# Optimization experiments

Measured on AMD Instinct MI355X. Metric: run time of the kernel, lower is better.

## Reference

```python
import jax, jax.numpy as jnp
import numpy as np

B, N, CH, DIM, SLOTS, ITERS, HID = 32, 4096, 256, 256, 11, 3, 512
EPS_ATTN = 1e-8
LN_EPS = 1e-3


def _ln(x, g, b):
    m = jnp.mean(x, axis=-1, keepdims=True)
    v = jnp.mean((x - m) ** 2, axis=-1, keepdims=True)
    return (x - m) * jax.lax.rsqrt(v + LN_EPS) * g + b


def setup_inputs() -> dict:
    key = jax.random.key(0)
    ks = jax.random.split(key, 16)
    s = lambda d: 1.0 / np.sqrt(d)
    return {
        "inputs": jax.random.normal(ks[0], (B, N, CH), jnp.float32),
        "noise": jax.random.normal(ks[1], (B, SLOTS, DIM), jnp.float32),
        "slots_mu": jax.random.uniform(ks[2], (1, 1, DIM), jnp.float32, -0.15, 0.15),
        "slots_log_sigma": jax.random.uniform(ks[3], (1, 1, DIM), jnp.float32, -0.15, 0.15),
        "Wq": jax.random.normal(ks[4], (DIM, DIM), jnp.float32) * s(DIM),
        "Wk": jax.random.normal(ks[5], (DIM, CH), jnp.float32) * s(CH),
        "Wv": jax.random.normal(ks[6], (DIM, CH), jnp.float32) * s(CH),
        "W_ih": jax.random.normal(ks[7], (3 * DIM, DIM), jnp.float32) * s(DIM),
        "W_hh": jax.random.normal(ks[8], (3 * DIM, DIM), jnp.float32) * s(DIM),
        "b_ih": jnp.zeros((3 * DIM,), jnp.float32),
        "b_hh": jnp.zeros((3 * DIM,), jnp.float32),
        "W1": jax.random.normal(ks[9], (HID, DIM), jnp.float32) * s(DIM),
        "b1": jnp.zeros((HID,), jnp.float32),
        "W2": jax.random.normal(ks[10], (DIM, HID), jnp.float32) * s(HID),
        "b2": jnp.zeros((DIM,), jnp.float32),
        "g_in": jnp.ones((CH,), jnp.float32), "be_in": jnp.zeros((CH,), jnp.float32),
        "g_sl": jnp.ones((DIM,), jnp.float32), "be_sl": jnp.zeros((DIM,), jnp.float32),
        "g_ff": jnp.ones((DIM,), jnp.float32), "be_ff": jnp.zeros((DIM,), jnp.float32),
    }


def reference(inputs, noise, slots_mu, slots_log_sigma, Wq, Wk, Wv, W_ih, W_hh,
              b_ih, b_hh, W1, b1, W2, b2, g_in, be_in, g_sl, be_sl, g_ff, be_ff):
    scale = DIM ** -0.5
    # reparameterized slot init: Normal(mu, exp(log_sigma))
    slots = slots_mu + jnp.exp(slots_log_sigma) * noise  # (B, S, D)
    x = _ln(inputs, g_in, be_in)
    k = jnp.einsum('bnc,dc->bnd', x, Wk)  # (B, N, D)
    v = jnp.einsum('bnc,dc->bnd', x, Wv)

    def gru(u, h):
        gi = u @ W_ih.T + b_ih
        gh = h @ W_hh.T + b_hh
        i_r, i_z, i_n = jnp.split(gi, 3, axis=-1)
        h_r, h_z, h_n = jnp.split(gh, 3, axis=-1)
        r = jax.nn.sigmoid(i_r + h_r)
        z = jax.nn.sigmoid(i_z + h_z)
        n = jnp.tanh(i_n + r * h_n)
        return (1.0 - z) * n + z * h

    for _ in range(ITERS):
        slots_prev = slots
        q = jnp.einsum('bid,ed->bie', _ln(slots, g_sl, be_sl), Wq)
        dots = jnp.einsum('bid,bjd->bij', q, k) * scale  # (B, S, N)
        attn = jax.nn.softmax(dots, axis=1) + EPS_ATTN   # competitive over slots
        attn = attn / jnp.sum(attn, axis=-1, keepdims=True)
        updates = jnp.einsum('bjd,bij->bid', v, attn)    # (B, S, D)
        slots = gru(updates.reshape(-1, DIM), slots_prev.reshape(-1, DIM)).reshape(B, -1, DIM)
        h = jax.nn.relu(_ln(slots, g_ff, be_ff) @ W1.T + b1)
        slots = slots + h @ W2.T + b2
    return slots
```

## Files before the change

kernel.cpp:

```cpp
#include <hip/hip_runtime.h>
#include <hip/hip_bf16.h>
#include <math.h>

typedef __bf16 bf16;
typedef __bf16 bf16x8 __attribute__((ext_vector_type(8)));
typedef float  f32x4  __attribute__((ext_vector_type(4)));

#define DEVI static __device__ __forceinline__

constexpr int B_ = 32, N_ = 4096, NS_ = 11, SP_ = 16, ITERS_ = 3;
constexpr int P_ = 32;
constexpr float LN_EPS_ = 1e-3f;
constexpr float EPS_ATTN_ = 1e-8f;

DEVI f32x4 mfma16(bf16x8 a, bf16x8 b, f32x4 c) {
  return __builtin_amdgcn_mfma_f32_16x16x32_bf16(a, b, c, 0, 0, 0);
}

DEVI float wsum64(float v) {
#pragma unroll
  for (int m = 32; m > 0; m >>= 1) v += __shfl_xor(v, m, 64);
  return v;
}

__global__ __launch_bounds__(256) void cast_weights(
    const float* __restrict__ Wq, const float* __restrict__ Wk,
    const float* __restrict__ Wv, const float* __restrict__ Wih,
    const float* __restrict__ Whh, const float* __restrict__ W1,
    const float* __restrict__ W2,
    bf16* __restrict__ cWkT, bf16* __restrict__ cWvT, bf16* __restrict__ cWq,
    bf16* __restrict__ cWih, bf16* __restrict__ cWhh, bf16* __restrict__ cW1,
    bf16* __restrict__ cW2) {
  const int idx = blockIdx.x * 256 + threadIdx.x;
  const int n0 = 256 * 256;
  const int n1 = n0 + 256 * 256;
  const int n2 = n1 + 256 * 256;
  const int n3 = n2 + 768 * 256;
  const int n4 = n3 + 768 * 256;
  const int n5 = n4 + 512 * 256;
  const int n6 = n5 + 256 * 512;
  if (idx < n0) {
    const int c = idx >> 8, d = idx & 255;
    cWkT[idx] = (bf16)Wk[d * 256 + c];
  } else if (idx < n1) {
    const int i = idx - n0; const int c = i >> 8, d = i & 255;
    cWvT[i] = (bf16)Wv[d * 256 + c];
  } else if (idx < n2) { const int i = idx - n1; cWq[i]  = (bf16)Wq[i];
  } else if (idx < n3) { const int i = idx - n2; cWih[i] = (bf16)Wih[i];
  } else if (idx < n4) { const int i = idx - n3; cWhh[i] = (bf16)Whh[i];
  } else if (idx < n5) { const int i = idx - n4; cW1[i]  = (bf16)W1[i];
  } else if (idx < n6) { const int i = idx - n5; cW2[i]  = (bf16)W2[i]; }
}

__global__ __launch_bounds__(256) void wfold_gemm(
    const bf16* __restrict__ Wih, const bf16* __restrict__ WvT,
    bf16* __restrict__ Wfold) {
  __shared__ bf16 At[32 * 256];
  const int mt = blockIdx.x, nt = blockIdx.y;
  const int tid = threadIdx.x, lane = tid & 63, wid = tid >> 6;
  const int l15 = lane & 15, gq = lane >> 4;
  const bf16* A = Wih + (size_t)mt * 32 * 256;
#pragma unroll
  for (int i = 0; i < 4; ++i) {
    const int idx = i * 256 + tid, row = idx >> 5, c = idx & 31;
    const bf16x8 v = *(const bf16x8*)(A + row * 256 + c * 8);
    const int byte = (row * 512 + c * 16) ^ ((row & 7) << 4);
    *(bf16x8*)((char*)At + byte) = v;
  }
  __syncthreads();
  const int wr = wid >> 1, wc = wid & 1;
  f32x4 acc[2] = {};
  for (int kk = 0; kk < 8; ++kk) {
    const int arow = wr * 16 + l15;
    const int byte = (arow * 512 + kk * 64 + gq * 16) ^ ((arow & 7) << 4);
    const bf16x8 af = *(const bf16x8*)((const char*)At + byte);
#pragma unroll
    for (int nn = 0; nn < 2; ++nn) {
      const bf16* wrow = WvT + (size_t)(nt * 64 + wc * 32 + nn * 16 + l15) * 256 + kk * 32 + gq * 8;
      acc[nn] = mfma16(af, *(const bf16x8*)wrow, acc[nn]);
    }
  }
#pragma unroll
  for (int nn = 0; nn < 2; ++nn)
#pragma unroll
    for (int r = 0; r < 4; ++r) {
      const int grow = mt * 32 + wr * 16 + gq * 4 + r;
      const int col = nt * 64 + wc * 32 + nn * 16 + l15;
      Wfold[(size_t)grow * 256 + col] = (bf16)acc[nn][r];
    }
}

__global__ __launch_bounds__(256) void init_slots(
    const float* __restrict__ mu, const float* __restrict__ lsig,
    const float* __restrict__ noise, float* __restrict__ slots,
    bf16* __restrict__ slots_bf) {
  const int idx = blockIdx.x * 256 + threadIdx.x;
  const int d = idx & 255;
  const float v = mu[d] + expf(lsig[d]) * noise[idx];
  slots[idx] = v;
  slots_bf[idx] = (bf16)v;
}

__global__ __launch_bounds__(256) void ln_castT(
    const float* __restrict__ inp, const float* __restrict__ g,
    const float* __restrict__ be, bf16* __restrict__ xhat,
    bf16* __restrict__ xhatT) {
  __shared__ bf16 Bt[256 * 128];
  const int mt = blockIdx.x;
  const int tid = threadIdx.x, lane = tid & 63, wid = tid >> 6;
  const int l15 = lane & 15, gq = lane >> 4;
  float4 gv[4], bv4[4];
#pragma unroll
  for (int u = 0; u < 4; ++u) {
    gv[u]  = ((const float4*)g)[l15 * 4 + u];
    bv4[u] = ((const float4*)be)[l15 * 4 + u];
  }
  const int c0 = l15 * 16;
  char* btlane = (char*)Bt + c0 * 256;
  for (int it8 = 0; it8 < 8; ++it8) {
    const int row = wid * 32 + it8 * 4 + gq;
    const size_t grow = (size_t)mt * 128 + row;
    const float4* rp = (const float4*)(inp + grow * 256 + l15 * 16);
    float4 x[4];
#pragma unroll
    for (int u = 0; u < 4; ++u) x[u] = rp[u];
    float s = 0.f, ss = 0.f;
#pragma unroll
    for (int u = 0; u < 4; ++u) {
      s += x[u].x + x[u].y + x[u].z + x[u].w;
      ss = fmaf(x[u].x, x[u].x, fmaf(x[u].y, x[u].y,
           fmaf(x[u].z, x[u].z, fmaf(x[u].w, x[u].w, ss))));
    }
#pragma unroll
    for (int m = 8; m > 0; m >>= 1) {
      s  += __shfl_xor(s,  m, 16);
      ss += __shfl_xor(ss, m, 16);
    }
    const float mean = s * (1.f / 256.f);
    const float rstd = rsqrtf(ss * (1.f / 256.f) - mean * mean + LN_EPS_);
    float y[16];
#pragma unroll
    for (int u = 0; u < 4; ++u) {
      y[u * 4 + 0] = (x[u].x - mean) * rstd * gv[u].x + bv4[u].x;
      y[u * 4 + 1] = (x[u].y - mean) * rstd * gv[u].y + bv4[u].y;
      y[u * 4 + 2] = (x[u].z - mean) * rstd * gv[u].z + bv4[u].z;
      y[u * 4 + 3] = (x[u].w - mean) * rstd * gv[u].w + bv4[u].w;
    }
    bf16x8 y0, y1;
#pragma unroll
    for (int e = 0; e < 8; ++e) { y0[e] = (bf16)y[e]; y1[e] = (bf16)y[8 + e]; }
    bf16* orow = xhat + grow * 256 + c0;
    *(bf16x8*)orow       = y0;
    *(bf16x8*)(orow + 8) = y1;
    const int roff = (row * 2) ^ c0;
#pragma unroll
    for (int j = 0; j < 8; ++j) {
      *(bf16*)(btlane + j * 256 + roff)         = y0[j];
      *(bf16*)(btlane + (8 + j) * 256 + roff)   = y1[j];
    }
  }
  __syncthreads();
  const int bidx = mt >> 5, jtile = (mt & 31) * 128;
#pragma unroll
  for (int i = 0; i < 16; ++i) {
    const int idx = i * 256 + tid;
    const int c = idx >> 4, j8 = (idx & 15) * 8;
    const bf16x8 v = *(const bf16x8*)((const char*)Bt +
                                      (c * 256 + ((j8 * 2) ^ (c & 0xF0))));
    *(bf16x8*)&xhatT[((size_t)(bidx * 256 + c)) * N_ + jtile + j8] = v;
  }
}

__global__ __launch_bounds__(256) void q_proj(
    const float* __restrict__ slots, const float* __restrict__ g,
    const float* __restrict__ be, const bf16* __restrict__ Wqb,
    const bf16* __restrict__ WkT, bf16* __restrict__ qpad) {
  const int i = blockIdx.x, b = blockIdx.y, t = threadIdx.x;
  bf16* out = qpad + (b * SP_ + i) * 256;
  if (i >= NS_) { out[t] = (bf16)0.f; return; }
  __shared__ float lnv[256], qd[256];
  __shared__ float red[8];
  const float x = slots[(b * NS_ + i) * 256 + t];
  float s = wsum64(x), ss = wsum64(x * x);
  const int lane = t & 63, w = t >> 6;
  if (lane == 0) { red[w] = s; red[4 + w] = ss; }
  __syncthreads();
  const float st = red[0] + red[1] + red[2] + red[3];
  const float qt = red[4] + red[5] + red[6] + red[7];
  const float mean = st / 256.f, var = qt / 256.f - mean * mean;
  const float rstd = rsqrtf(var + LN_EPS_);
  lnv[t] = (x - mean) * rstd * g[t] + be[t];
  __syncthreads();
  {
    float acc = 0.f;
    const bf16* wr = Wqb + (size_t)t * 256;
    for (int it = 0; it < 32; ++it) {
      const bf16x8 wv = *(const bf16x8*)(wr + it * 8);
      const float* u = &lnv[it * 8];
#pragma unroll
      for (int e = 0; e < 8; ++e) acc += (float)wv[e] * u[e];
    }
    qd[t] = acc;
  }
  __syncthreads();
  {
    float acc = 0.f;
    const bf16* wr = WkT + (size_t)t * 256;
    for (int it = 0; it < 32; ++it) {
      const bf16x8 wv = *(const bf16x8*)(wr + it * 8);
      const float* u = &qd[it * 8];
#pragma unroll
      for (int e = 0; e < 8; ++e) acc += (float)wv[e] * u[e];
    }
    out[t] = (bf16)(acc * 0.0625f);
  }
}

__global__ __launch_bounds__(256) void attn_part(
    const bf16* __restrict__ xhat, const bf16* __restrict__ xhatT,
    const bf16* __restrict__ qpad,
    float* __restrict__ num_part, float* __restrict__ den_part) {
  const int part = blockIdx.x, b = blockIdx.y;
  const int lane = threadIdx.x & 63, wid = threadIdx.x >> 6;
  const int l15 = lane & 15, gq = lane >> 4;
  const int jbase = part * 128 + wid * 32;
  const bf16* qrow = qpad + ((size_t)(b * SP_ + l15)) * 256;
  const bf16* kbase = xhat + ((size_t)(b * N_ + jbase)) * 256;
  const bf16* vtb = xhatT + ((size_t)b * 256) * N_ + jbase + gq * 8;
  __shared__ float nsw[2][4096];
  __shared__ float dens[4][16];

  bf16x8 bq[8];
#pragma unroll
  for (int kk = 0; kk < 8; ++kk)
    bq[kk] = *(const bf16x8*)(qrow + kk * 32 + gq * 8);
  bf16x8 v0[8];
#pragma unroll
  for (int dblk = 0; dblk < 8; ++dblk)
    v0[dblk] = *(const bf16x8*)(vtb + (size_t)(dblk * 16 + l15) * N_);

  float denacc = 0.f;
  float p0[4], p1[4];
#pragma unroll
  for (int T = 0; T < 2; ++T) {
    const bf16* krow = kbase + (size_t)(T * 16 + l15) * 256;
    f32x4 d = {0.f, 0.f, 0.f, 0.f};
#pragma unroll
    for (int kk = 0; kk < 8; ++kk) {
      const bf16x8 ak = *(const bf16x8*)(krow + kk * 32 + gq * 8);
      d = mfma16(ak, bq[kk], d);
    }
#pragma unroll
    for (int r = 0; r < 4; ++r) {
      float vmax = (l15 < NS_) ? d[r] : -1e30f;
#pragma unroll
      for (int mm = 8; mm > 0; mm >>= 1) vmax = fmaxf(vmax, __shfl_xor(vmax, mm, 16));
      const float e = (l15 < NS_) ? expf(d[r] - vmax) : 0.f;
      float ssum = e;
#pragma unroll
      for (int mm = 8; mm > 0; mm >>= 1) ssum += __shfl_xor(ssum, mm, 16);
      const float p = (l15 < NS_) ? (e / ssum + EPS_ATTN_) : 0.f;
      if (T == 0) p0[r] = p; else p1[r] = p;
      denacc += p;
    }
  }
  bf16x8 v1[8];
#pragma unroll
  for (int dblk = 0; dblk < 8; ++dblk)
    v1[dblk] = *(const bf16x8*)(vtb + (size_t)((8 + dblk) * 16 + l15) * N_);
  bf16x8 ap;
#pragma unroll
  for (int e = 0; e < 8; ++e) {
    const int srcl = l15 + ((2 * (gq & 1) + (e >> 2)) << 4);
    const float va = __shfl(p0[e & 3], srcl, 64);
    const float vb = __shfl(p1[e & 3], srcl, 64);
    ap[e] = (bf16)((gq < 2) ? va : vb);
  }
  f32x4 accN[16];
  __builtin_amdgcn_s_setprio(1);
#pragma unroll
  for (int dblk = 0; dblk < 8; ++dblk) {
    f32x4 z = {0.f, 0.f, 0.f, 0.f};
    accN[dblk] = mfma16(ap, v0[dblk], z);
  }
#pragma unroll
  for (int dblk = 0; dblk < 8; ++dblk) {
    f32x4 z = {0.f, 0.f, 0.f, 0.f};
    accN[8 + dblk] = mfma16(ap, v1[dblk], z);
  }
  __builtin_amdgcn_s_setprio(0);
  if (wid < 2) {
#pragma unroll
    for (int dblk = 0; dblk < 16; ++dblk)
#pragma unroll
      for (int r = 0; r < 4; ++r) {
        const int idx = (((4 * gq + r) * 256) + dblk * 16 + l15) ^ (gq << 4);
        nsw[wid][idx] = accN[dblk][r];
      }
  }
  __syncthreads();
  if (wid >= 2) {
#pragma unroll
    for (int dblk = 0; dblk < 16; ++dblk)
#pragma unroll
      for (int r = 0; r < 4; ++r) {
        const int idx = (((4 * gq + r) * 256) + dblk * 16 + l15) ^ (gq << 4);
        nsw[wid - 2][idx] += accN[dblk][r];
      }
  }
  float dtot = denacc + __shfl_xor(denacc, 16, 64);
  dtot += __shfl_xor(dtot, 32, 64);
  if (lane < 16) dens[wid][l15] = dtot;
  __syncthreads();
  const int t = threadIdx.x;
  if (t < NS_)
    den_part[(b * P_ + part) * NS_ + t] =
        dens[0][t] + dens[1][t] + dens[2][t] + dens[3][t];
  for (int r = 0; r < NS_; ++r) {
    const int swz = ((r >> 2) & 3) << 4;
    num_part[((size_t)((b * P_ + part) * NS_ + r)) * 256 + t] =
        nsw[0][(r * 256 + t) ^ swz] + nsw[1][(r * 256 + t) ^ swz];
  }
}

__global__ __launch_bounds__(256) void u0_reduce(
    const float* __restrict__ num_part, const float* __restrict__ den_part,
    bf16* __restrict__ u0b) {
  const int row = blockIdx.x, t = threadIdx.x;
  const int b = row / NS_, i = row % NS_;
  float nsum = 0.f;
  for (int p = 0; p < P_; ++p)
    nsum += num_part[((size_t)((b * P_ + p) * NS_ + i)) * 256 + t];
  float den = 0.f;
  for (int p = 0; p < P_; ++p) den += den_part[(b * P_ + p) * NS_ + i];
  u0b[(size_t)row * 256 + t] = (bf16)(nsum / den);
}

__global__ __launch_bounds__(256) void gates_gemm(
    const bf16* __restrict__ u0b, const bf16* __restrict__ hb,
    const bf16* __restrict__ Wfold, const bf16* __restrict__ Whh,
    float* __restrict__ gi, float* __restrict__ gh) {
  __shared__ bf16 At[32 * 256];
  const int mt = blockIdx.x, nt = blockIdx.y;
  const bool isI = nt < 12;
  const int ntile = isI ? nt : nt - 12;
  const bf16* A = (isI ? u0b : hb) + (size_t)mt * 32 * 256;
  const bf16* W = isI ? Wfold : Whh;
  float* out = isI ? gi : gh;
  const int tid = threadIdx.x, lane = tid & 63, wid = tid >> 6;
  const int l15 = lane & 15, gq = lane >> 4;
#pragma unroll
  for (int i = 0; i < 4; ++i) {
    const int idx = i * 256 + tid, row = idx >> 5, c = idx & 31;
    const bf16x8 v = *(const bf16x8*)(A + row * 256 + c * 8);
    const int byte = (row * 512 + c * 16) ^ ((row & 7) << 4);
    *(bf16x8*)((char*)At + byte) = v;
  }
  __syncthreads();
  const int wr = wid >> 1, wc = wid & 1;
  f32x4 acc[2] = {};
  for (int kk = 0; kk < 8; ++kk) {
    const int arow = wr * 16 + l15;
    const int byte = (arow * 512 + kk * 64 + gq * 16) ^ ((arow & 7) << 4);
    const bf16x8 af = *(const bf16x8*)((const char*)At + byte);
#pragma unroll
    for (int nn = 0; nn < 2; ++nn) {
      const bf16* wrow = W + (size_t)(ntile * 64 + wc * 32 + nn * 16 + l15) * 256 + kk * 32 + gq * 8;
      acc[nn] = mfma16(af, *(const bf16x8*)wrow, acc[nn]);
    }
  }
#pragma unroll
  for (int nn = 0; nn < 2; ++nn)
#pragma unroll
    for (int r = 0; r < 4; ++r) {
      const int grow = mt * 32 + wr * 16 + gq * 4 + r;
      const int col = ntile * 64 + wc * 32 + nn * 16 + l15;
      out[(size_t)grow * 768 + col] = acc[nn][r];
    }
}

__global__ __launch_bounds__(256) void gru_ew(
    const float* __restrict__ gi, const float* __restrict__ gh,
    const float* __restrict__ bih, const float* __restrict__ bhh,
    const float* __restrict__ slots_f, const float* __restrict__ gff,
    const float* __restrict__ beff, float* __restrict__ hn_out,
    bf16* __restrict__ ln_out) {
  const int row = blockIdx.x, t = threadIdx.x;
  __shared__ float red[8];
  const size_t g0 = (size_t)row * 768;
  const float ir = gi[g0 + t]       + bih[t];
  const float hr = gh[g0 + t]       + bhh[t];
  const float iz = gi[g0 + 256 + t] + bih[256 + t];
  const float hz = gh[g0 + 256 + t] + bhh[256 + t];
  const float inn = gi[g0 + 512 + t] + bih[512 + t];
  const float hnn = gh[g0 + 512 + t] + bhh[512 + t];
  const float h = slots_f[(size_t)row * 256 + t];
  const float r = 1.f / (1.f + expf(-(ir + hr)));
  const float z = 1.f / (1.f + expf(-(iz + hz)));
  const float n = tanhf(inn + r * hnn);
  const float hn = (1.f - z) * n + z * h;
  hn_out[(size_t)row * 256 + t] = hn;
  float s = wsum64(hn), ss = wsum64(hn * hn);
  const int lane = t & 63, w = t >> 6;
  if (lane == 0) { red[w] = s; red[4 + w] = ss; }
  __syncthreads();
  const float st = red[0] + red[1] + red[2] + red[3];
  const float qt = red[4] + red[5] + red[6] + red[7];
  const float mean = st / 256.f, var = qt / 256.f - mean * mean;
  const float rstd = rsqrtf(var + LN_EPS_);
  ln_out[(size_t)row * 256 + t] = (bf16)((hn - mean) * rstd * gff[t] + beff[t]);
}

__global__ __launch_bounds__(256) void w1_gemm(
    const bf16* __restrict__ lnb, const bf16* __restrict__ W1,
    const float* __restrict__ b1, bf16* __restrict__ h1b) {
  __shared__ bf16 At[32 * 256];
  const int mt = blockIdx.x, nt = blockIdx.y;
  const int tid = threadIdx.x, lane = tid & 63, wid = tid >> 6;
  const int l15 = lane & 15, gq = lane >> 4;
  const bf16* A = lnb + (size_t)mt * 32 * 256;
#pragma unroll
  for (int i = 0; i < 4; ++i) {
    const int idx = i * 256 + tid, row = idx >> 5, c = idx & 31;
    const bf16x8 v = *(const bf16x8*)(A + row * 256 + c * 8);
    const int byte = (row * 512 + c * 16) ^ ((row & 7) << 4);
    *(bf16x8*)((char*)At + byte) = v;
  }
  __syncthreads();
  const int wr = wid >> 1, wc = wid & 1;
  f32x4 acc[2] = {};
  for (int kk = 0; kk < 8; ++kk) {
    const int arow = wr * 16 + l15;
    const int byte = (arow * 512 + kk * 64 + gq * 16) ^ ((arow & 7) << 4);
    const bf16x8 af = *(const bf16x8*)((const char*)At + byte);
#pragma unroll
    for (int nn = 0; nn < 2; ++nn) {
      const bf16* wrow = W1 + (size_t)(nt * 64 + wc * 32 + nn * 16 + l15) * 256 + kk * 32 + gq * 8;
      acc[nn] = mfma16(af, *(const bf16x8*)wrow, acc[nn]);
    }
  }
#pragma unroll
  for (int nn = 0; nn < 2; ++nn)
#pragma unroll
    for (int r = 0; r < 4; ++r) {
      const int grow = mt * 32 + wr * 16 + gq * 4 + r;
      const int col = nt * 64 + wc * 32 + nn * 16 + l15;
      h1b[(size_t)grow * 512 + col] = (bf16)fmaxf(acc[nn][r] + b1[col], 0.f);
    }
}

__global__ __launch_bounds__(256) void w2_gemm(
    const bf16* __restrict__ h1b, const bf16* __restrict__ W2,
    const float* __restrict__ b2, const float* __restrict__ hn_in,
    float* __restrict__ sout, bf16* __restrict__ sbf) {
  __shared__ bf16 At[32 * 512];
  const int mt = blockIdx.x, nt = blockIdx.y;
  const int tid = threadIdx.x, lane = tid & 63, wid = tid >> 6;
  const int l15 = lane & 15, gq = lane >> 4;
  const bf16* A = h1b + (size_t)mt * 32 * 512;
#pragma unroll
  for (int i = 0; i < 8; ++i) {
    const int idx = i * 256 + tid, row = idx >> 6, c = idx & 63;
    const bf16x8 v = *(const bf16x8*)(A + row * 512 + c * 8);
    const int byte = (row * 1024 + c * 16) ^ ((row & 7) << 4);
    *(bf16x8*)((char*)At + byte) = v;
  }
  __syncthreads();
  const int wr = wid >> 1, wc = wid & 1;
  f32x4 acc[2] = {};
  for (int kk = 0; kk < 16; ++kk) {
    const int arow = wr * 16 + l15;
    const int byte = (arow * 1024 + kk * 64 + gq * 16) ^ ((arow & 7) << 4);
    const bf16x8 af = *(const bf16x8*)((const char*)At + byte);
#pragma unroll
    for (int nn = 0; nn < 2; ++nn) {
      const bf16* wrow = W2 + (size_t)(nt * 64 + wc * 32 + nn * 16 + l15) * 512 + kk * 32 + gq * 8;
      acc[nn] = mfma16(af, *(const bf16x8*)wrow, acc[nn]);
    }
  }
#pragma unroll
  for (int nn = 0; nn < 2; ++nn)
#pragma unroll
    for (int r = 0; r < 4; ++r) {
      const int grow = mt * 32 + wr * 16 + gq * 4 + r;
      const int col = nt * 64 + wc * 32 + nn * 16 + l15;
      const float v = hn_in[(size_t)grow * 256 + col] + acc[nn][r] + b2[col];
      sout[(size_t)grow * 256 + col] = v;
      sbf[(size_t)grow * 256 + col] = (bf16)v;
    }
}

extern "C" void kernel_launch(void* const* d_in, const int* in_sizes, int n_in,
                              void* d_out, int out_size, void* d_ws, size_t ws_size,
                              hipStream_t stream) {
  const float* inputs = (const float*)d_in[0];
  const float* noise  = (const float*)d_in[1];
  const float* mu     = (const float*)d_in[2];
  const float* lsig   = (const float*)d_in[3];
  const float* Wq     = (const float*)d_in[4];
  const float* Wk     = (const float*)d_in[5];
  const float* Wv     = (const float*)d_in[6];
  const float* Wih    = (const float*)d_in[7];
  const float* Whh    = (const float*)d_in[8];
  const float* bih    = (const float*)d_in[9];
  const float* bhh    = (const float*)d_in[10];
  const float* W1     = (const float*)d_in[11];
  const float* b1     = (const float*)d_in[12];
  const float* W2     = (const float*)d_in[13];
  const float* b2     = (const float*)d_in[14];
  const float* gin    = (const float*)d_in[15];
  const float* bein   = (const float*)d_in[16];
  const float* gsl    = (const float*)d_in[17];
  const float* besl   = (const float*)d_in[18];
  const float* gff    = (const float*)d_in[19];
  const float* beff   = (const float*)d_in[20];

  char* ws = (char*)d_ws;
  size_t off = 0;
  auto alloc = [&](size_t bytes) -> void* {
    void* p = ws + off;
    off += (bytes + 255) & ~(size_t)255;
    return p;
  };
  bf16*  xhat    = (bf16*) alloc((size_t)B_ * N_ * 256 * 2);
  bf16*  xhatT   = (bf16*) alloc((size_t)B_ * 256 * N_ * 2);
  bf16*  qpad    = (bf16*) alloc((size_t)B_ * SP_ * 256 * 2);
  bf16*  cWkT    = (bf16*) alloc(256 * 256 * 2);
  bf16*  cWvT    = (bf16*) alloc(256 * 256 * 2);
  bf16*  cWq     = (bf16*) alloc(256 * 256 * 2);
  bf16*  cWih    = (bf16*) alloc(768 * 256 * 2);
  bf16*  cWhh    = (bf16*) alloc(768 * 256 * 2);
  bf16*  cW1     = (bf16*) alloc(512 * 256 * 2);
  bf16*  cW2     = (bf16*) alloc(256 * 512 * 2);
  bf16*  Wfold   = (bf16*) alloc(768 * 256 * 2);
  float* slots   = (float*)alloc((size_t)352 * 256 * 4);
  bf16*  slots_bf= (bf16*) alloc((size_t)352 * 256 * 2);
  float* numpart = (float*)alloc((size_t)B_ * P_ * NS_ * 256 * 4);
  float* denpart = (float*)alloc((size_t)B_ * P_ * NS_ * 4);
  bf16*  u0b     = (bf16*) alloc((size_t)352 * 256 * 2);
  float* gi      = (float*)alloc((size_t)352 * 768 * 4);
  float* gh      = (float*)alloc((size_t)352 * 768 * 4);
  float* hn_f    = (float*)alloc((size_t)352 * 256 * 4);
  bf16*  ln_b    = (bf16*) alloc((size_t)352 * 256 * 2);
  bf16*  h1b     = (bf16*) alloc((size_t)352 * 512 * 2);
  (void)ws_size; (void)in_sizes; (void)n_in; (void)out_size;

  cast_weights<<<3328, 256, 0, stream>>>(Wq, Wk, Wv, Wih, Whh, W1, W2,
                                         cWkT, cWvT, cWq, cWih, cWhh, cW1, cW2);
  wfold_gemm<<<dim3(24, 4), 256, 0, stream>>>(cWih, cWvT, Wfold);
  init_slots<<<352, 256, 0, stream>>>(mu, lsig, noise, slots, slots_bf);
  ln_castT<<<1024, 256, 0, stream>>>(inputs, gin, bein, xhat, xhatT);
  for (int it = 0; it < ITERS_; ++it) {
    q_proj<<<dim3(SP_, B_), 256, 0, stream>>>(slots, gsl, besl, cWq, cWkT, qpad);
    attn_part<<<dim3(P_, B_), 256, 0, stream>>>(xhat, xhatT, qpad, numpart, denpart);
    u0_reduce<<<352, 256, 0, stream>>>(numpart, denpart, u0b);
    gates_gemm<<<dim3(11, 24), 256, 0, stream>>>(u0b, slots_bf, Wfold, cWhh, gi, gh);
    gru_ew<<<352, 256, 0, stream>>>(gi, gh, bih, bhh, slots, gff, beff, hn_f, ln_b);
    w1_gemm<<<dim3(11, 8), 256, 0, stream>>>(ln_b, cW1, b1, h1b);
    float* sout = (it == ITERS_ - 1) ? (float*)d_out : slots;
    w2_gemm<<<dim3(11, 4), 256, 0, stream>>>(h1b, cW2, b2, hn_f, sout, slots_bf);
  }
}
```

Before: 288.6 us.

## Fuse slot reduce, GRU gates, LayerNorm and MLP into one slot_update kernel

Replaces the per-iteration chain of u0_reduce, gates_gemm, gru_ew, w1_gemm and w2_gemm with a single kernel. Each 512-thread block handles 16 slot rows end to end: it reduces the attention partials, runs the fused input and hidden gate GEMMs, applies the GRU, the LayerNorm and both MLP layers, keeping intermediates in shared memory. The aim is to remove four launches per iteration and the global round-trips through the gi, gh, hn, ln and h1 buffers. The cost is a grid of only 22 blocks, so every block re-reads all the weights from L2 and the partial reduction runs with far less parallelism than before.

```diff
diff --git a/kernel.cpp b/kernel.cpp
--- a/kernel.cpp
+++ b/kernel.cpp
@@ -92,13 +92,10 @@
 
 __global__ __launch_bounds__(256) void init_slots(
     const float* __restrict__ mu, const float* __restrict__ lsig,
-    const float* __restrict__ noise, float* __restrict__ slots,
-    bf16* __restrict__ slots_bf) {
+    const float* __restrict__ noise, float* __restrict__ slots) {
   const int idx = blockIdx.x * 256 + threadIdx.x;
   const int d = idx & 255;
-  const float v = mu[d] + expf(lsig[d]) * noise[idx];
-  slots[idx] = v;
-  slots_bf[idx] = (bf16)v;
+  slots[idx] = mu[d] + expf(lsig[d]) * noise[idx];
 }
 
 __global__ __launch_bounds__(256) void ln_castT(
@@ -323,171 +320,158 @@
   }
 }
 
-__global__ __launch_bounds__(256) void u0_reduce(
+__global__ __launch_bounds__(512) void slot_update(
     const float* __restrict__ num_part, const float* __restrict__ den_part,
-    bf16* __restrict__ u0b) {
-  const int row = blockIdx.x, t = threadIdx.x;
-  const int b = row / NS_, i = row % NS_;
-  float nsum = 0.f;
-  for (int p = 0; p < P_; ++p)
-    nsum += num_part[((size_t)((b * P_ + p) * NS_ + i)) * 256 + t];
-  float den = 0.f;
-  for (int p = 0; p < P_; ++p) den += den_part[(b * P_ + p) * NS_ + i];
-  u0b[(size_t)row * 256 + t] = (bf16)(nsum / den);
-}
-
-__global__ __launch_bounds__(256) void gates_gemm(
-    const bf16* __restrict__ u0b, const bf16* __restrict__ hb,
     const bf16* __restrict__ Wfold, const bf16* __restrict__ Whh,
-    float* __restrict__ gi, float* __restrict__ gh) {
-  __shared__ bf16 At[32 * 256];
-  const int mt = blockIdx.x, nt = blockIdx.y;
-  const bool isI = nt < 12;
-  const int ntile = isI ? nt : nt - 12;
-  const bf16* A = (isI ? u0b : hb) + (size_t)mt * 32 * 256;
-  const bf16* W = isI ? Wfold : Whh;
-  float* out = isI ? gi : gh;
+    const float* __restrict__ bih, const float* __restrict__ bhh,
+    const float* __restrict__ slots_f, const bf16* __restrict__ W1,
+    const float* __restrict__ b1, const bf16* __restrict__ W2,
+    const float* __restrict__ b2, const float* __restrict__ gff,
+    const float* __restrict__ beff, float* __restrict__ sout) {
+  const int mt = blockIdx.x;
   const int tid = threadIdx.x, lane = tid & 63, wid = tid >> 6;
   const int l15 = lane & 15, gq = lane >> 4;
-#pragma unroll
-  for (int i = 0; i < 4; ++i) {
-    const int idx = i * 256 + tid, row = idx >> 5, c = idx & 31;
-    const bf16x8 v = *(const bf16x8*)(A + row * 256 + c * 8);
-    const int byte = (row * 512 + c * 16) ^ ((row & 7) << 4);
-    *(bf16x8*)((char*)At + byte) = v;
-  }
-  __syncthreads();
-  const int wr = wid >> 1, wc = wid & 1;
-  f32x4 acc[2] = {};
+  __shared__ bf16 Au[16 * 256];
+  __shared__ bf16 Ah[16 * 256];
+  __shared__ float hn_s[16 * 256];
+  __shared__ bf16 ln_s2[16 * 256];
+  __shared__ bf16 h1_s2[16 * 512];
+  __shared__ float den_s[16];
+  if (tid < 16) {
+    const int grow = mt * 16 + tid;
+    const int b = grow / NS_, sl = grow - b * NS_;
+    float den = 0.f;
+    for (int p = 0; p < P_; ++p) den += den_part[(b * P_ + p) * NS_ + sl];
+    den_s[tid] = den;
+  }
+  __syncthreads();
+#pragma unroll
+  for (int i = 0; i < 8; ++i) {
+    const int idx = i * 512 + tid;
+    const int row = idx >> 8, c = idx & 255;
+    const int grow = mt * 16 + row;
+    const int b = grow / NS_, sl = grow - b * NS_;
+    float nsum = 0.f;
+    for (int p = 0; p < P_; ++p)
+      nsum += num_part[((size_t)((b * P_ + p) * NS_ + sl)) * 256 + c];
+    const int byte = (row * 512 + c * 2) ^ ((row & 7) << 4);
+    *(bf16*)((char*)Au + byte) = (bf16)(nsum / den_s[row]);
+    *(bf16*)((char*)Ah + byte) = (bf16)slots_f[(size_t)grow * 256 + c];
+  }
+  __syncthreads();
+  const int wcol = wid * 32;
+  f32x4 acc[12] = {};
   for (int kk = 0; kk < 8; ++kk) {
-    const int arow = wr * 16 + l15;
-    const int byte = (arow * 512 + kk * 64 + gq * 16) ^ ((arow & 7) << 4);
-    const bf16x8 af = *(const bf16x8*)((const char*)At + byte);
-#pragma unroll
-    for (int nn = 0; nn < 2; ++nn) {
-      const bf16* wrow = W + (size_t)(ntile * 64 + wc * 32 + nn * 16 + l15) * 256 + kk * 32 + gq * 8;
-      acc[nn] = mfma16(af, *(const bf16x8*)wrow, acc[nn]);
-    }
-  }
-#pragma unroll
-  for (int nn = 0; nn < 2; ++nn)
+    const int abyte = (l15 * 512 + kk * 64 + gq * 16) ^ ((l15 & 7) << 4);
+    const bf16x8 au = *(const bf16x8*)((const char*)Au + abyte);
+    const bf16x8 ah = *(const bf16x8*)((const char*)Ah + abyte);
+#pragma unroll
+    for (int ggt = 0; ggt < 3; ++ggt)
+#pragma unroll
+      for (int tc = 0; tc < 2; ++tc) {
+        const int wrow = ggt * 256 + wcol + tc * 16 + l15;
+        const bf16x8 wfi = *(const bf16x8*)(Wfold + (size_t)wrow * 256 + kk * 32 + gq * 8);
+        const bf16x8 whv = *(const bf16x8*)(Whh   + (size_t)wrow * 256 + kk * 32 + gq * 8);
+        acc[(ggt * 2 + 0) * 2 + tc] = mfma16(au, wfi, acc[(ggt * 2 + 0) * 2 + tc]);
+        acc[(ggt * 2 + 1) * 2 + tc] = mfma16(ah, whv, acc[(ggt * 2 + 1) * 2 + tc]);
+      }
+  }
+#pragma unroll
+  for (int tc = 0; tc < 2; ++tc) {
+    const int col = wcol + tc * 16 + l15;
+    const float bir = bih[col],        bhr = bhh[col];
+    const float biz = bih[256 + col],  bhz = bhh[256 + col];
+    const float bin = bih[512 + col],  bhn = bhh[512 + col];
 #pragma unroll
     for (int r = 0; r < 4; ++r) {
-      const int grow = mt * 32 + wr * 16 + gq * 4 + r;
-      const int col = ntile * 64 + wc * 32 + nn * 16 + l15;
-      out[(size_t)grow * 768 + col] = acc[nn][r];
-    }
-}
-
-__global__ __launch_bounds__(256) void gru_ew(
-    const float* __restrict__ gi, const float* __restrict__ gh,
-    const float* __restrict__ bih, const float* __restrict__ bhh,
-    const float* __restrict__ slots_f, const float* __restrict__ gff,
-    const float* __restrict__ beff, float* __restrict__ hn_out,
-    bf16* __restrict__ ln_out) {
-  const int row = blockIdx.x, t = threadIdx.x;
-  __shared__ float red[8];
-  const size_t g0 = (size_t)row * 768;
-  const float ir = gi[g0 + t]       + bih[t];
-  const float hr = gh[g0 + t]       + bhh[t];
-  const float iz = gi[g0 + 256 + t] + bih[256 + t];
-  const float hz = gh[g0 + 256 + t] + bhh[256 + t];
-  const float inn = gi[g0 + 512 + t] + bih[512 + t];
-  const float hnn = gh[g0 + 512 + t] + bhh[512 + t];
-  const float h = slots_f[(size_t)row * 256 + t];
-  const float r = 1.f / (1.f + expf(-(ir + hr)));
-  const float z = 1.f / (1.f + expf(-(iz + hz)));
-  const float n = tanhf(inn + r * hnn);
-  const float hn = (1.f - z) * n + z * h;
-  hn_out[(size_t)row * 256 + t] = hn;
-  float s = wsum64(hn), ss = wsum64(hn * hn);
-  const int lane = t & 63, w = t >> 6;
-  if (lane == 0) { red[w] = s; red[4 + w] = ss; }
-  __syncthreads();
-  const float st = red[0] + red[1] + red[2] + red[3];
-  const float qt = red[4] + red[5] + red[6] + red[7];
-  const float mean = st / 256.f, var = qt / 256.f - mean * mean;
-  const float rstd = rsqrtf(var + LN_EPS_);
-  ln_out[(size_t)row * 256 + t] = (bf16)((hn - mean) * rstd * gff[t] + beff[t]);
-}
-
-__global__ __launch_bounds__(256) void w1_gemm(
-    const bf16* __restrict__ lnb, const bf16* __restrict__ W1,
-    const float* __restrict__ b1, bf16* __restrict__ h1b) {
-  __shared__ bf16 At[32 * 256];
-  const int mt = blockIdx.x, nt = blockIdx.y;
-  const int tid = threadIdx.x, lane = tid & 63, wid = tid >> 6;
-  const int l15 = lane & 15, gq = lane >> 4;
-  const bf16* A = lnb + (size_t)mt * 32 * 256;
-#pragma unroll
-  for (int i = 0; i < 4; ++i) {
-    const int idx = i * 256 + tid, row = idx >> 5, c = idx & 31;
-    const bf16x8 v = *(const bf16x8*)(A + row * 256 + c * 8);
-    const int byte = (row * 512 + c * 16) ^ ((row & 7) << 4);
-    *(bf16x8*)((char*)At + byte) = v;
-  }
-  __syncthreads();
-  const int wr = wid >> 1, wc = wid & 1;
-  f32x4 acc[2] = {};
-  for (int kk = 0; kk < 8; ++kk) {
-    const int arow = wr * 16 + l15;
-    const int byte = (arow * 512 + kk * 64 + gq * 16) ^ ((arow & 7) << 4);
-    const bf16x8 af = *(const bf16x8*)((const char*)At + byte);
-#pragma unroll
-    for (int nn = 0; nn < 2; ++nn) {
-      const bf16* wrow = W1 + (size_t)(nt * 64 + wc * 32 + nn * 16 + l15) * 256 + kk * 32 + gq * 8;
-      acc[nn] = mfma16(af, *(const bf16x8*)wrow, acc[nn]);
-    }
-  }
-#pragma unroll
-  for (int nn = 0; nn < 2; ++nn)
-#pragma unroll
-    for (int r = 0; r < 4; ++r) {
-      const int grow = mt * 32 + wr * 16 + gq * 4 + r;
-      const int col = nt * 64 + wc * 32 + nn * 16 + l15;
-      h1b[(size_t)grow * 512 + col] = (bf16)fmaxf(acc[nn][r] + b1[col], 0.f);
-    }
-}
-
-__global__ __launch_bounds__(256) void w2_gemm(
-    const bf16* __restrict__ h1b, const bf16* __restrict__ W2,
-    const float* __restrict__ b2, const float* __restrict__ hn_in,
-    float* __restrict__ sout, bf16* __restrict__ sbf) {
-  __shared__ bf16 At[32 * 512];
-  const int mt = blockIdx.x, nt = blockIdx.y;
-  const int tid = threadIdx.x, lane = tid & 63, wid = tid >> 6;
-  const int l15 = lane & 15, gq = lane >> 4;
-  const bf16* A = h1b + (size_t)mt * 32 * 512;
-#pragma unroll
-  for (int i = 0; i < 8; ++i) {
-    const int idx = i * 256 + tid, row = idx >> 6, c = idx & 63;
-    const bf16x8 v = *(const bf16x8*)(A + row * 512 + c * 8);
-    const int byte = (row * 1024 + c * 16) ^ ((row & 7) << 4);
-    *(bf16x8*)((char*)At + byte) = v;
-  }
-  __syncthreads();
-  const int wr = wid >> 1, wc = wid & 1;
-  f32x4 acc[2] = {};
-  for (int kk = 0; kk < 16; ++kk) {
-    const int arow = wr * 16 + l15;
-    const int byte = (arow * 1024 + kk * 64 + gq * 16) ^ ((arow & 7) << 4);
-    const bf16x8 af = *(const bf16x8*)((const char*)At + byte);
-#pragma unroll
-    for (int nn = 0; nn < 2; ++nn) {
-      const bf16* wrow = W2 + (size_t)(nt * 64 + wc * 32 + nn * 16 + l15) * 512 + kk * 32 + gq * 8;
-      acc[nn] = mfma16(af, *(const bf16x8*)wrow, acc[nn]);
-    }
-  }
-#pragma unroll
-  for (int nn = 0; nn < 2; ++nn)
-#pragma unroll
-    for (int r = 0; r < 4; ++r) {
-      const int grow = mt * 32 + wr * 16 + gq * 4 + r;
-      const int col = nt * 64 + wc * 32 + nn * 16 + l15;
-      const float v = hn_in[(size_t)grow * 256 + col] + acc[nn][r] + b2[col];
-      sout[(size_t)grow * 256 + col] = v;
-      sbf[(size_t)grow * 256 + col] = (bf16)v;
-    }
+      const int row = gq * 4 + r;
+      const int grow = mt * 16 + row;
+      const float ir = acc[0 * 2 + tc][r] + bir;
+      const float hr = acc[1 * 2 + tc][r] + bhr;
+      const float iz = acc[2 * 2 + tc][r] + biz;
+      const float hz = acc[3 * 2 + tc][r] + bhz;
+      const float inn = acc[4 * 2 + tc][r] + bin;
+      const float hnn = acc[5 * 2 + tc][r] + bhn;
+      const float h = slots_f[(size_t)grow * 256 + col];
+      const float rg = 1.f / (1.f + expf(-(ir + hr)));
+      const float zg = 1.f / (1.f + expf(-(iz + hz)));
+      const float ng = tanhf(inn + rg * hnn);
+      hn_s[row * 256 + col] = (1.f - zg) * ng + zg * h;
+    }
+  }
+  __syncthreads();
+  {
+    const int row = tid >> 5, sub = tid & 31;
+    float s = 0.f, ss = 0.f;
+    float v[8];
+#pragma unroll
+    for (int e = 0; e < 8; ++e) {
+      v[e] = hn_s[row * 256 + sub * 8 + e];
+      s += v[e]; ss = fmaf(v[e], v[e], ss);
+    }
+#pragma unroll
+    for (int m = 16; m > 0; m >>= 1) {
+      s  += __shfl_xor(s,  m, 32);
+      ss += __shfl_xor(ss, m, 32);
+    }
+    const float mean = s * (1.f / 256.f);
+    const float rstd = rsqrtf(ss * (1.f / 256.f) - mean * mean + LN_EPS_);
+#pragma unroll
+    for (int e = 0; e < 8; ++e) {
+      const int c = sub * 8 + e;
+      const float lv = (v[e] - mean) * rstd * gff[c] + beff[c];
+      const int byte = (row * 512 + c * 2) ^ ((row & 7) << 4);
+      *(bf16*)((char*)ln_s2 + byte) = (bf16)lv;
+    }
+  }
+  __syncthreads();
+  {
+    f32x4 a4[4] = {};
+    for (int kk = 0; kk < 8; ++kk) {
+      const int abyte = (l15 * 512 + kk * 64 + gq * 16) ^ ((l15 & 7) << 4);
+      const bf16x8 af = *(const bf16x8*)((const char*)ln_s2 + abyte);
+#pragma unroll
+      for (int nn = 0; nn < 4; ++nn) {
+        const int wrow = wid * 64 + nn * 16 + l15;
+        const bf16x8 bf = *(const bf16x8*)(W1 + (size_t)wrow * 256 + kk * 32 + gq * 8);
+        a4[nn] = mfma16(af, bf, a4[nn]);
+      }
+    }
+#pragma unroll
+    for (int nn = 0; nn < 4; ++nn)
+#pragma unroll
+      for (int r = 0; r < 4; ++r) {
+        const int row = gq * 4 + r;
+        const int col = wid * 64 + nn * 16 + l15;
+        const float hv = fmaxf(a4[nn][r] + b1[col], 0.f);
+        const int byte = (row * 1024 + col * 2) ^ ((row & 7) << 4);
+        *(bf16*)((char*)h1_s2 + byte) = (bf16)hv;
+      }
+  }
+  __syncthreads();
+  {
+    f32x4 a2[2] = {};
+    for (int kk = 0; kk < 16; ++kk) {
+      const int abyte = (l15 * 1024 + kk * 64 + gq * 16) ^ ((l15 & 7) << 4);
+      const bf16x8 af = *(const bf16x8*)((const char*)h1_s2 + abyte);
+#pragma unroll
+      for (int nn = 0; nn < 2; ++nn) {
+        const int wrow = wid * 32 + nn * 16 + l15;
+        const bf16x8 bf = *(const bf16x8*)(W2 + (size_t)wrow * 512 + kk * 32 + gq * 8);
+        a2[nn] = mfma16(af, bf, a2[nn]);
+      }
+    }
+#pragma unroll
+    for (int nn = 0; nn < 2; ++nn)
+#pragma unroll
+      for (int r = 0; r < 4; ++r) {
+        const int row = gq * 4 + r;
+        const int col = wid * 32 + nn * 16 + l15;
+        const int grow = mt * 16 + row;
+        sout[(size_t)grow * 256 + col] =
+            hn_s[row * 256 + col] + a2[nn][r] + b2[col];
+      }
+  }
 }
 
 extern "C" void kernel_launch(void* const* d_in, const int* in_sizes, int n_in,
@@ -534,30 +518,20 @@
   bf16*  cW2     = (bf16*) alloc(256 * 512 * 2);
   bf16*  Wfold   = (bf16*) alloc(768 * 256 * 2);
   float* slots   = (float*)alloc((size_t)352 * 256 * 4);
-  bf16*  slots_bf= (bf16*) alloc((size_t)352 * 256 * 2);
   float* numpart = (float*)alloc((size_t)B_ * P_ * NS_ * 256 * 4);
   float* denpart = (float*)alloc((size_t)B_ * P_ * NS_ * 4);
-  bf16*  u0b     = (bf16*) alloc((size_t)352 * 256 * 2);
-  float* gi      = (float*)alloc((size_t)352 * 768 * 4);
-  float* gh      = (float*)alloc((size_t)352 * 768 * 4);
-  float* hn_f    = (float*)alloc((size_t)352 * 256 * 4);
-  bf16*  ln_b    = (bf16*) alloc((size_t)352 * 256 * 2);
-  bf16*  h1b     = (bf16*) alloc((size_t)352 * 512 * 2);
   (void)ws_size; (void)in_sizes; (void)n_in; (void)out_size;
 
   cast_weights<<<3328, 256, 0, stream>>>(Wq, Wk, Wv, Wih, Whh, W1, W2,
                                          cWkT, cWvT, cWq, cWih, cWhh, cW1, cW2);
   wfold_gemm<<<dim3(24, 4), 256, 0, stream>>>(cWih, cWvT, Wfold);
-  init_slots<<<352, 256, 0, stream>>>(mu, lsig, noise, slots, slots_bf);
+  init_slots<<<352, 256, 0, stream>>>(mu, lsig, noise, slots);
   ln_castT<<<1024, 256, 0, stream>>>(inputs, gin, bein, xhat, xhatT);
   for (int it = 0; it < ITERS_; ++it) {
     q_proj<<<dim3(SP_, B_), 256, 0, stream>>>(slots, gsl, besl, cWq, cWkT, qpad);
     attn_part<<<dim3(P_, B_), 256, 0, stream>>>(xhat, xhatT, qpad, numpart, denpart);
-    u0_reduce<<<352, 256, 0, stream>>>(numpart, denpart, u0b);
-    gates_gemm<<<dim3(11, 24), 256, 0, stream>>>(u0b, slots_bf, Wfold, cWhh, gi, gh);
-    gru_ew<<<352, 256, 0, stream>>>(gi, gh, bih, bhh, slots, gff, beff, hn_f, ln_b);
-    w1_gemm<<<dim3(11, 8), 256, 0, stream>>>(ln_b, cW1, b1, h1b);
     float* sout = (it == ITERS_ - 1) ? (float*)d_out : slots;
-    w2_gemm<<<dim3(11, 4), 256, 0, stream>>>(h1b, cW2, b2, hn_f, sout, slots_bf);
-  }
-}
+    slot_update<<<22, 512, 0, stream>>>(numpart, denpart, Wfold, cWhh,
+        bih, bhh, slots, cW1, b1, cW2, b2, gff, beff, sout);
+  }
+}
```

After: 349.7 us. +21.2%, slower.
